# Kernel optimization log

Hardware: AMD Instinct MI355X
Metric: run time of the kernel (lower is better)

## Reference

```python
import jax, jax.numpy as jnp
import numpy as np

N_USERS = 100000
N_GAMES = 50000
D = 128
E = 1600000


def setup_inputs() -> dict:
    key = jax.random.key(0)
    k1, k2, k3, k4 = jax.random.split(key, 4)
    user_h = jax.random.normal(k1, (N_USERS, D), dtype=jnp.float32)
    game_h = jax.random.normal(k2, (N_GAMES, D), dtype=jnp.float32)
    src_idx = jax.random.randint(k3, (E,), 0, N_USERS, dtype=jnp.int64)
    dst_idx = jax.random.randint(k4, (E,), 0, N_GAMES, dtype=jnp.int64)
    return {"user_h": user_h, "game_h": game_h, "src_idx": src_idx, "dst_idx": dst_idx}


def reference(user_h, game_h, src_idx, dst_idx):
    # DGL fn.u_dot_v: gather src/dst node features along the edge list,
    # then per-edge dot product. Output shape [E, 1] (DGL keeps last dim).
    u = user_h[src_idx]          # [E, D] gather
    v = game_h[dst_idx]          # [E, D] gather
    score = jnp.sum(u * v, axis=-1, keepdims=True)  # [E, 1]
    return score
```

## Files before the change

kernel.cpp:

```cpp
#include <hip/hip_runtime.h>


#define DIM 128
#define NB 64
#define CAP 28160
#define BPB 782
#define N_USERS_C 100000u
#define EPB_A 4096

__device__ inline unsigned bf16rn(float f) {
    unsigned x = __float_as_uint(f);
    return (x + 0x7FFFu + ((x >> 16) & 1u)) >> 16;
}

__global__ void __launch_bounds__(256) prep_fused(
    const float* __restrict__ user_h, const float* __restrict__ game_h,
    const int* __restrict__ src_idx, const int* __restrict__ dst_idx, int E,
    unsigned* __restrict__ cursors, uint2* __restrict__ records,
    unsigned* __restrict__ pos,
    uint4* __restrict__ user_bf, uint4* __restrict__ game_bf,
    int nscat, int nublk, int nu8, int ng8)
{
    __shared__ unsigned hist[NB];
    __shared__ unsigned base_s[NB];
    __shared__ unsigned lcur[NB];
    int bid = blockIdx.x;
    int tid = threadIdx.x;

    if (bid >= nscat) {
        const float* in;
        uint4* outp;
        int i, n8;
        if (bid < nscat + nublk) {
            i = (bid - nscat) * 256 + tid;  n8 = nu8;  in = user_h;  outp = user_bf;
        } else {
            i = (bid - nscat - nublk) * 256 + tid;  n8 = ng8;  in = game_h;  outp = game_bf;
        }
        if (i < n8) {
            const float4* in4 = (const float4*)in;
            float4 a = in4[2 * i];
            float4 b = in4[2 * i + 1];
            uint4 o;
            o.x = bf16rn(a.x) | (bf16rn(a.y) << 16);
            o.y = bf16rn(a.z) | (bf16rn(a.w) << 16);
            o.z = bf16rn(b.x) | (bf16rn(b.y) << 16);
            o.w = bf16rn(b.z) | (bf16rn(b.w) << 16);
            outp[i] = o;
        }
        return;
    }

    long long start = (long long)bid * EPB_A;
    unsigned ss[16], dd[16];

    #pragma unroll
    for (int k = 0; k < 16; ++k) {
        long long e = start + k * 256 + tid;
        bool v = (e < E);
        ss[k] = v ? (unsigned)src_idx[e] : 0xFFFFFFFFu;
        dd[k] = v ? (unsigned)dst_idx[e] : 0u;
    }

    if (tid < NB) hist[tid] = 0u;
    __syncthreads();

    #pragma unroll
    for (int k = 0; k < 16; ++k) {
        if (ss[k] != 0xFFFFFFFFu) {
            unsigned b = (ss[k] * (unsigned)NB) / N_USERS_C;
            atomicAdd(&hist[b], 1u);
        }
    }
    __syncthreads();

    if (tid < NB) {
        base_s[tid] = atomicAdd(&cursors[tid * 32], hist[tid]);
        lcur[tid] = 0u;
    }
    __syncthreads();

    #pragma unroll
    for (int k = 0; k < 16; ++k) {
        if (ss[k] != 0xFFFFFFFFu) {
            unsigned s = ss[k], d = dd[k];
            unsigned b = (s * (unsigned)NB) / N_USERS_C;
            unsigned r = atomicAdd(&lcur[b], 1u);
            unsigned pr = base_s[b] + r;
            long long e = start + k * 256 + tid;
            if (pr < (unsigned)CAP) {
                uint2 rec;
                rec.x = s | ((d & 0x7FFFu) << 17);
                rec.y = (d >> 15);
                records[(size_t)b * CAP + pr] = rec;
                pos[e] = b * (unsigned)CAP + pr;
            } else {
                pos[e] = 0xFFFFFFFFu;
            }
        }
    }
}

__device__ inline float dot8_bf16(uint4 a, uint4 b) {
    float s;
    s  = __uint_as_float(a.x << 16)          * __uint_as_float(b.x << 16);
    s += __uint_as_float(a.x & 0xFFFF0000u)  * __uint_as_float(b.x & 0xFFFF0000u);
    s += __uint_as_float(a.y << 16)          * __uint_as_float(b.y << 16);
    s += __uint_as_float(a.y & 0xFFFF0000u)  * __uint_as_float(b.y & 0xFFFF0000u);
    s += __uint_as_float(a.z << 16)          * __uint_as_float(b.z << 16);
    s += __uint_as_float(a.z & 0xFFFF0000u)  * __uint_as_float(b.z & 0xFFFF0000u);
    s += __uint_as_float(a.w << 16)          * __uint_as_float(b.w << 16);
    s += __uint_as_float(a.w & 0xFFFF0000u)  * __uint_as_float(b.w & 0xFFFF0000u);
    return s;
}

__global__ void __launch_bounds__(256) edge_dot_bucketed_bf16(
    const uint4* __restrict__ user_bf, const uint4* __restrict__ game_bf,
    const unsigned* __restrict__ cursors, const uint2* __restrict__ records,
    float* __restrict__ res)
{
    int bid = blockIdx.x;
    int x = bid & 7;
    int n = bid >> 3;
    int bq = n / BPB;
    int chunk = n - bq * BPB;
    int b = x + 8 * bq;

    int count = (int)cursors[b * 32];
    if (count > CAP) count = CAP;
    const uint2* __restrict__ rec = records + (size_t)b * CAP;
    float* __restrict__ rout = res + (size_t)b * CAP;

    int g    = threadIdx.x >> 4;
    int lane = threadIdx.x & 15;

    for (int j0 = chunk * 32; j0 < count; j0 += BPB * 32) {
        int j = j0 + 2 * g;
        if (j >= count) continue;
        bool has1 = (j + 1 < count);

        uint2 r0 = rec[j];
        uint2 r1 = has1 ? rec[j + 1] : r0;

        unsigned s0 = r0.x & 0x1FFFFu;
        unsigned d0 = ((r0.x >> 17) & 0x7FFFu) | ((r0.y & 1u) << 15);
        unsigned s1 = r1.x & 0x1FFFFu;
        unsigned d1 = ((r1.x >> 17) & 0x7FFFu) | ((r1.y & 1u) << 15);

        uint4 ua = user_bf[(size_t)s0 * 16 + lane];
        uint4 va = game_bf[(size_t)d0 * 16 + lane];
        uint4 ub = user_bf[(size_t)s1 * 16 + lane];
        uint4 vb = game_bf[(size_t)d1 * 16 + lane];

        float sum0 = dot8_bf16(ua, va);
        float sum1 = dot8_bf16(ub, vb);

        sum0 += __shfl_xor(sum0, 1);  sum1 += __shfl_xor(sum1, 1);
        sum0 += __shfl_xor(sum0, 2);  sum1 += __shfl_xor(sum1, 2);
        sum0 += __shfl_xor(sum0, 4);  sum1 += __shfl_xor(sum1, 4);
        sum0 += __shfl_xor(sum0, 8);  sum1 += __shfl_xor(sum1, 8);

        if (lane == 0) {
            if (has1) {
                *(float2*)(rout + j) = make_float2(sum0, sum1);
            } else {
                rout[j] = sum0;
            }
        }
    }
}

__global__ void __launch_bounds__(256) scatter_out(
    const unsigned* __restrict__ pos, const float* __restrict__ res,
    float* __restrict__ out, int E)
{
    int i4 = blockIdx.x * blockDim.x + threadIdx.x;
    int n4 = E >> 2;
    if (i4 < n4) {
        uint4 p = ((const uint4*)pos)[i4];
        float4 o;
        o.x = (p.x != 0xFFFFFFFFu) ? res[p.x] : 0.0f;
        o.y = (p.y != 0xFFFFFFFFu) ? res[p.y] : 0.0f;
        o.z = (p.z != 0xFFFFFFFFu) ? res[p.z] : 0.0f;
        o.w = (p.w != 0xFFFFFFFFu) ? res[p.w] : 0.0f;
        ((float4*)out)[i4] = o;
    } else if (i4 == n4) {
        for (int e = n4 * 4; e < E; ++e) {
            unsigned p = pos[e];
            out[e] = (p != 0xFFFFFFFFu) ? res[p] : 0.0f;
        }
    }
}

__global__ void __launch_bounds__(256) edge_dot_kernel(
    const float* __restrict__ user_h,
    const float* __restrict__ game_h,
    const int* __restrict__ src_idx,
    const int* __restrict__ dst_idx,
    float* __restrict__ out,
    int E)
{
    int tid  = blockIdx.x * blockDim.x + threadIdx.x;
    int g    = tid >> 4;
    int lane = tid & 15;
    long long e0 = (long long)g * 2;
    if (e0 >= E) return;
    bool has1 = (e0 + 1 < E);

    int s0 = src_idx[e0];
    int d0 = dst_idx[e0];
    int s1 = has1 ? src_idx[e0 + 1] : s0;
    int d1 = has1 ? dst_idx[e0 + 1] : d0;

    const float4* __restrict__ u0 = (const float4*)(user_h + (size_t)s0 * DIM);
    const float4* __restrict__ v0 = (const float4*)(game_h + (size_t)d0 * DIM);
    const float4* __restrict__ u1 = (const float4*)(user_h + (size_t)s1 * DIM);
    const float4* __restrict__ v1 = (const float4*)(game_h + (size_t)d1 * DIM);

    float4 ua0 = u0[lane];
    float4 ua1 = u0[lane + 16];
    float4 va0 = v0[lane];
    float4 va1 = v0[lane + 16];
    float4 ub0 = u1[lane];
    float4 ub1 = u1[lane + 16];
    float4 vb0 = v1[lane];
    float4 vb1 = v1[lane + 16];

    float sum0 = ua0.x * va0.x + ua0.y * va0.y + ua0.z * va0.z + ua0.w * va0.w
               + ua1.x * va1.x + ua1.y * va1.y + ua1.z * va1.z + ua1.w * va1.w;
    float sum1 = ub0.x * vb0.x + ub0.y * vb0.y + ub0.z * vb0.z + ub0.w * vb0.w
               + ub1.x * vb1.x + ub1.y * vb1.y + ub1.z * vb1.z + ub1.w * vb1.w;

    sum0 += __shfl_xor(sum0, 1);  sum1 += __shfl_xor(sum1, 1);
    sum0 += __shfl_xor(sum0, 2);  sum1 += __shfl_xor(sum1, 2);
    sum0 += __shfl_xor(sum0, 4);  sum1 += __shfl_xor(sum1, 4);
    sum0 += __shfl_xor(sum0, 8);  sum1 += __shfl_xor(sum1, 8);

    if (lane == 0) {
        out[e0] = sum0;
        if (has1) out[e0 + 1] = sum1;
    }
}

extern "C" void kernel_launch(void* const* d_in, const int* in_sizes, int n_in,
                              void* d_out, int out_size, void* d_ws, size_t ws_size,
                              hipStream_t stream) {
    const float* user_h  = (const float*)d_in[0];
    const float* game_h  = (const float*)d_in[1];
    const int*   src_idx = (const int*)d_in[2];
    const int*   dst_idx = (const int*)d_in[3];
    float*       out     = (float*)d_out;

    int E       = in_sizes[2];
    int n_user  = in_sizes[0];
    int n_game  = in_sizes[1];

    size_t rec_bytes = (size_t)NB * CAP * sizeof(uint2);
    size_t res_bytes = (size_t)NB * CAP * sizeof(float);
    size_t pos_bytes = (size_t)E * sizeof(unsigned);
    size_t ws_full   = 8192 + rec_bytes + (size_t)n_user * 2 + (size_t)n_game * 2
                     + pos_bytes + res_bytes;

    if (ws_size < ws_full || E > (1 << 21)) {
        long long nblocks = ((long long)E + 31) / 32;
        edge_dot_kernel<<<(int)nblocks, 256, 0, stream>>>(
            user_h, game_h, src_idx, dst_idx, out, E);
        return;
    }

    char* p = (char*)d_ws;
    unsigned* cursors = (unsigned*)p;                 p += 8192;
    uint2*    records = (uint2*)p;                    p += rec_bytes;
    uint4*    user_bf = (uint4*)p;                    p += (size_t)n_user * 2;
    uint4*    game_bf = (uint4*)p;                    p += (size_t)n_game * 2;
    unsigned* pos     = (unsigned*)p;                 p += pos_bytes;
    float*    res     = (float*)p;

    hipMemsetAsync(cursors, 0, 8192, stream);

    int nu8   = n_user / 8;
    int ng8   = n_game / 8;
    int nscat = (E + EPB_A - 1) / EPB_A;
    int nublk = (nu8 + 255) / 256;
    int ngblk = (ng8 + 255) / 256;

    prep_fused<<<nscat + nublk + ngblk, 256, 0, stream>>>(
        user_h, game_h, src_idx, dst_idx, E,
        cursors, records, pos, user_bf, game_bf,
        nscat, nublk, nu8, ng8);

    edge_dot_bucketed_bf16<<<NB * BPB, 256, 0, stream>>>(
        user_bf, game_bf, cursors, records, res);

    int n4 = E / 4;
    scatter_out<<<(n4 + 256) / 256, 256, 0, stream>>>(pos, res, out, E);
}
```

Baseline: 102.5 us.

## Compress bucket records to 32 bits and stage scatter writes in LDS

Edge records are shrunk from 8 to 4 bytes by storing each source index as an offset from its bucket base and packing it with the destination index. The scatter kernel now collects the first records of each bucket in shared memory and writes them out in contiguous runs, so global stores coalesce. This halves record traffic in both the prep and dot kernels. It adds 32KB of LDS per block, which may lower occupancy, and adds guard conditions on input sizes.

```diff
diff --git a/kernel.cpp b/kernel.cpp
--- a/kernel.cpp
+++ b/kernel.cpp
@@ -5,8 +5,8 @@
 #define NB 64
 #define CAP 28160
 #define BPB 782
-#define N_USERS_C 100000u
 #define EPB_A 4096
+#define LCAP 128
 
 __device__ inline unsigned bf16rn(float f) {
     unsigned x = __float_as_uint(f);
@@ -16,7 +16,8 @@
 __global__ void __launch_bounds__(256) prep_fused(
     const float* __restrict__ user_h, const float* __restrict__ game_h,
     const int* __restrict__ src_idx, const int* __restrict__ dst_idx, int E,
-    unsigned* __restrict__ cursors, uint2* __restrict__ records,
+    unsigned n_users,
+    unsigned* __restrict__ cursors, unsigned* __restrict__ records,
     unsigned* __restrict__ pos,
     uint4* __restrict__ user_bf, uint4* __restrict__ game_bf,
     int nscat, int nublk, int nu8, int ng8)
@@ -24,6 +25,7 @@
     __shared__ unsigned hist[NB];
     __shared__ unsigned base_s[NB];
     __shared__ unsigned lcur[NB];
+    __shared__ unsigned stage[NB][LCAP];
     int bid = blockIdx.x;
     int tid = threadIdx.x;
 
@@ -67,7 +69,7 @@
     #pragma unroll
     for (int k = 0; k < 16; ++k) {
         if (ss[k] != 0xFFFFFFFFu) {
-            unsigned b = (ss[k] * (unsigned)NB) / N_USERS_C;
+            unsigned b = (ss[k] * (unsigned)NB) / n_users;
             atomicAdd(&hist[b], 1u);
         }
     }
@@ -83,20 +85,33 @@
     for (int k = 0; k < 16; ++k) {
         if (ss[k] != 0xFFFFFFFFu) {
             unsigned s = ss[k], d = dd[k];
-            unsigned b = (s * (unsigned)NB) / N_USERS_C;
+            unsigned b = (s * (unsigned)NB) / n_users;
+            unsigned sbase = (b * n_users + (unsigned)NB - 1u) / (unsigned)NB;
+            unsigned rec = (s - sbase) | (d << 11);
             unsigned r = atomicAdd(&lcur[b], 1u);
-            unsigned pr = base_s[b] + r;
+            unsigned slot = base_s[b] + r;
             long long e = start + k * 256 + tid;
-            if (pr < (unsigned)CAP) {
-                uint2 rec;
-                rec.x = s | ((d & 0x7FFFu) << 17);
-                rec.y = (d >> 15);
-                records[(size_t)b * CAP + pr] = rec;
-                pos[e] = b * (unsigned)CAP + pr;
+            if (slot < (unsigned)CAP) {
+                pos[e] = b * (unsigned)CAP + slot;
+                if (r < (unsigned)LCAP) stage[b][r] = rec;
+                else records[(size_t)b * CAP + slot] = rec;
             } else {
                 pos[e] = 0xFFFFFFFFu;
             }
         }
+    }
+    __syncthreads();
+
+    int wid  = tid >> 6;
+    int lane = tid & 63;
+    for (int b = wid; b < NB; b += 4) {
+        unsigned n  = lcur[b]; if (n > (unsigned)LCAP) n = (unsigned)LCAP;
+        unsigned bs = base_s[b];
+        unsigned lim = (bs < (unsigned)CAP) ? ((unsigned)CAP - bs) : 0u;
+        if (n > lim) n = lim;
+        unsigned gbase = (unsigned)b * (unsigned)CAP + bs;
+        for (unsigned i = lane; i < n; i += 64)
+            records[gbase + i] = stage[b][i];
     }
 }
 
@@ -115,8 +130,8 @@
 
 __global__ void __launch_bounds__(256) edge_dot_bucketed_bf16(
     const uint4* __restrict__ user_bf, const uint4* __restrict__ game_bf,
-    const unsigned* __restrict__ cursors, const uint2* __restrict__ records,
-    float* __restrict__ res)
+    const unsigned* __restrict__ cursors, const unsigned* __restrict__ records,
+    unsigned n_users, float* __restrict__ res)
 {
     int bid = blockIdx.x;
     int x = bid & 7;
@@ -127,8 +142,9 @@
 
     int count = (int)cursors[b * 32];
     if (count > CAP) count = CAP;
-    const uint2* __restrict__ rec = records + (size_t)b * CAP;
+    const unsigned* __restrict__ rec = records + (size_t)b * CAP;
     float* __restrict__ rout = res + (size_t)b * CAP;
+    unsigned sbase = ((unsigned)b * n_users + (unsigned)NB - 1u) / (unsigned)NB;
 
     int g    = threadIdx.x >> 4;
     int lane = threadIdx.x & 15;
@@ -138,13 +154,14 @@
         if (j >= count) continue;
         bool has1 = (j + 1 < count);
 
-        uint2 r0 = rec[j];
-        uint2 r1 = has1 ? rec[j + 1] : r0;
-
-        unsigned s0 = r0.x & 0x1FFFFu;
-        unsigned d0 = ((r0.x >> 17) & 0x7FFFu) | ((r0.y & 1u) << 15);
-        unsigned s1 = r1.x & 0x1FFFFu;
-        unsigned d1 = ((r1.x >> 17) & 0x7FFFu) | ((r1.y & 1u) << 15);
+        uint2 rr = *(const uint2*)(rec + j);
+        unsigned r0 = rr.x;
+        unsigned r1 = has1 ? rr.y : rr.x;
+
+        unsigned s0 = sbase + (r0 & 0x7FFu);
+        unsigned d0 = r0 >> 11;
+        unsigned s1 = sbase + (r1 & 0x7FFu);
+        unsigned d1 = r1 >> 11;
 
         uint4 ua = user_bf[(size_t)s0 * 16 + lane];
         uint4 va = game_bf[(size_t)d0 * 16 + lane];
@@ -253,14 +270,22 @@
     int E       = in_sizes[2];
     int n_user  = in_sizes[0];
     int n_game  = in_sizes[1];
-
-    size_t rec_bytes = (size_t)NB * CAP * sizeof(uint2);
+    unsigned n_users = (unsigned)(n_user / DIM);
+    unsigned n_games = (unsigned)(n_game / DIM);
+
+    size_t rec_bytes = (size_t)NB * CAP * sizeof(unsigned);
     size_t res_bytes = (size_t)NB * CAP * sizeof(float);
     size_t pos_bytes = (size_t)E * sizeof(unsigned);
     size_t ws_full   = 8192 + rec_bytes + (size_t)n_user * 2 + (size_t)n_game * 2
                      + pos_bytes + res_bytes;
 
-    if (ws_size < ws_full || E > (1 << 21)) {
+    bool ok = (ws_size >= ws_full)
+           && (E <= 1650000)
+           && (n_users > 0) && (n_users <= (unsigned)NB * 2047u)
+           && (n_games <= 65536u)
+           && (n_user % (DIM) == 0) && (n_game % (DIM) == 0);
+
+    if (!ok) {
         long long nblocks = ((long long)E + 31) / 32;
         edge_dot_kernel<<<(int)nblocks, 256, 0, stream>>>(
             user_h, game_h, src_idx, dst_idx, out, E);
@@ -269,7 +294,7 @@
 
     char* p = (char*)d_ws;
     unsigned* cursors = (unsigned*)p;                 p += 8192;
-    uint2*    records = (uint2*)p;                    p += rec_bytes;
+    unsigned* records = (unsigned*)p;                 p += rec_bytes;
     uint4*    user_bf = (uint4*)p;                    p += (size_t)n_user * 2;
     uint4*    game_bf = (uint4*)p;                    p += (size_t)n_game * 2;
     unsigned* pos     = (unsigned*)p;                 p += pos_bytes;
@@ -284,12 +309,12 @@
     int ngblk = (ng8 + 255) / 256;
 
     prep_fused<<<nscat + nublk + ngblk, 256, 0, stream>>>(
-        user_h, game_h, src_idx, dst_idx, E,
+        user_h, game_h, src_idx, dst_idx, E, n_users,
         cursors, records, pos, user_bf, game_bf,
         nscat, nublk, nu8, ng8);
 
     edge_dot_bucketed_bf16<<<NB * BPB, 256, 0, stream>>>(
-        user_bf, game_bf, cursors, records, res);
+        user_bf, game_bf, cursors, records, n_users, res);
 
     int n4 = E / 4;
     scatter_out<<<(n4 + 256) / 256, 256, 0, stream>>>(pos, res, out, E);
```

Result: faster. 95.79 us (-6.5%).
